# Optimization experiments

Hardware: AMD Instinct MI355X
Metric: run time of the kernel (lower is better)

## Reference

```python
import jax, jax.numpy as jnp
import numpy as np

N_NODES = 50000
N_EDGES = 800000
NODE_DIM = 64
MSG_DIM = 64
EDGE_DIM = 4
ROUNDS = 2


def setup_inputs() -> dict:
    key = jax.random.key(0)
    ks = jax.random.split(key, 10)
    in_dim = 2 * NODE_DIM + EDGE_DIM  # cat([src hv, dst hv, he])
    return {
        "hv": jax.random.normal(ks[0], (N_NODES, NODE_DIM), dtype=jnp.float32),
        "he": jax.random.uniform(ks[1], (N_EDGES, EDGE_DIM), dtype=jnp.float32),
        "W_msg": jax.random.normal(ks[2], (ROUNDS, in_dim, MSG_DIM), dtype=jnp.float32) * 0.05,
        "b_msg": jax.random.normal(ks[3], (ROUNDS, MSG_DIM), dtype=jnp.float32) * 0.05,
        "W_ih": jax.random.normal(ks[4], (ROUNDS, MSG_DIM, 3 * NODE_DIM), dtype=jnp.float32) * 0.05,
        "W_hh": jax.random.normal(ks[5], (ROUNDS, NODE_DIM, 3 * NODE_DIM), dtype=jnp.float32) * 0.05,
        "b_ih": jax.random.normal(ks[6], (ROUNDS, 3 * NODE_DIM), dtype=jnp.float32) * 0.05,
        "b_hh": jax.random.normal(ks[7], (ROUNDS, 3 * NODE_DIM), dtype=jnp.float32) * 0.05,
        "src": jax.random.randint(ks[8], (N_EDGES,), 0, N_NODES, dtype=jnp.int64)
        if jax.config.jax_enable_x64 else jax.random.randint(ks[8], (N_EDGES,), 0, N_NODES).astype(jnp.int32),
        "dst": jax.random.randint(ks[9], (N_EDGES,), 0, N_NODES).astype(jnp.int32),
    }


def gru_cell(a, h, W_ih, W_hh, b_ih, b_hh):
    # torch.nn.GRUCell math; gate order (r, z, n) along the 3H axis
    gi = a @ W_ih + b_ih   # [N, 3H]
    gh = h @ W_hh + b_hh   # [N, 3H]
    i_r, i_z, i_n = jnp.split(gi, 3, axis=1)
    h_r, h_z, h_n = jnp.split(gh, 3, axis=1)
    r = jax.nn.sigmoid(i_r + h_r)
    z = jax.nn.sigmoid(i_z + h_z)
    n = jnp.tanh(i_n + r * h_n)
    return (1.0 - z) * n + z * h


def reference(hv, he, W_msg, b_msg, W_ih, W_hh, b_ih, b_hh, src, dst):
    # GraphProp.forward: per-round gather -> message MLP -> scatter-sum -> GRU update
    N = hv.shape[0]
    src = src.astype(jnp.int32)
    dst = dst.astype(jnp.int32)
    rounds = W_msg.shape[0]
    for t in range(rounds):
        # dgmg_msg: m = cat([src hv, dst hv, he])  [E, 2*D+E_dim]
        m_in = jnp.concatenate([hv[src], hv[dst], he], axis=1)
        msg = m_in @ W_msg[t] + b_msg[t]  # message_funcs[t] (Linear + Identity)
        # dgmg_reduce: sum of inbound messages per destination node
        a = jax.ops.segment_sum(msg, dst, num_segments=N)  # [N, MSG_DIM]
        hv = gru_cell(a, hv, W_ih[t], W_hh[t], b_ih[t], b_hh[t])
    return hv
```

## Files before the change

kernel.cpp:

```cpp
#include <hip/hip_runtime.h>

#define N_NODES 50000
#define N_EDGES 800000
#define D 64
#define EDIM 4
#define IN_DIM 132
#define H3 192
#define PAD 72


__global__ void k_count(const int* __restrict__ dst, int* __restrict__ deg) {
    int e = blockIdx.x * blockDim.x + threadIdx.x;
    if (e < N_EDGES) atomicAdd(&deg[dst[e]], 1);
}

__global__ __launch_bounds__(256) void k_scan1(const int* __restrict__ deg,
                                               int* __restrict__ offsets,
                                               int* __restrict__ bsum) {
    __shared__ int sm[256];
    int tid = threadIdx.x;
    int i = blockIdx.x * 256 + tid;
    int x = (i < N_NODES) ? deg[i] : 0;
    sm[tid] = x;
    __syncthreads();
    for (int s = 1; s < 256; s <<= 1) {
        int v = (tid >= s) ? sm[tid - s] : 0;
        __syncthreads();
        sm[tid] += v;
        __syncthreads();
    }
    if (i < N_NODES) offsets[i] = sm[tid] - x;
    if (tid == 255) bsum[blockIdx.x] = sm[255];
}

__global__ __launch_bounds__(256) void k_scan2(const int* __restrict__ bsum,
                                               int* __restrict__ boff, int nblk) {
    __shared__ int sm[256];
    int tid = threadIdx.x;
    int x = (tid < nblk) ? bsum[tid] : 0;
    sm[tid] = x;
    __syncthreads();
    for (int s = 1; s < 256; s <<= 1) {
        int v = (tid >= s) ? sm[tid - s] : 0;
        __syncthreads();
        sm[tid] += v;
        __syncthreads();
    }
    if (tid < nblk) boff[tid] = sm[tid] - x;
}

__global__ __launch_bounds__(256) void k_scan3(int* __restrict__ offsets,
                                               const int* __restrict__ boff) {
    int i = blockIdx.x * 256 + threadIdx.x;
    if (i < N_NODES) offsets[i] += boff[blockIdx.x];
}

__global__ void k_fill(const int* __restrict__ src, const int* __restrict__ dst,
                       const int* __restrict__ offsets, int* __restrict__ cursor,
                       int* __restrict__ csr_src, int* __restrict__ csr_eid) {
    int e = blockIdx.x * blockDim.x + threadIdx.x;
    if (e < N_EDGES) {
        int d = dst[e];
        int pos = offsets[d] + atomicAdd(&cursor[d], 1);
        csr_src[pos] = src[e];
        csr_eid[pos] = e;
    }
}


template <int ROUND>
__global__ __launch_bounds__(256) void k_reduce(const float* __restrict__ hv,
                                                const float* __restrict__ he,
                                                const int* __restrict__ csr_src,
                                                const int* __restrict__ csr_eid,
                                                const int* __restrict__ offsets,
                                                const int* __restrict__ deg,
                                                float* __restrict__ S,
                                                float* __restrict__ Hsum) {
    int wave = (blockIdx.x * blockDim.x + threadIdx.x) >> 6;
    if (wave >= N_NODES) return;
    int lane = threadIdx.x & 63;
    int g = lane >> 4;
    int c = lane & 15;
    const int off = offsets[wave];
    const int cnt = deg[wave];
    float4 acc = make_float4(0.f, 0.f, 0.f, 0.f);
    float4 hacc = make_float4(0.f, 0.f, 0.f, 0.f);
    for (int e = g; e < cnt; e += 4) {
        int sn = csr_src[off + e];
        float4 v = ((const float4*)(hv + (size_t)sn * D))[c];
        acc.x += v.x; acc.y += v.y; acc.z += v.z; acc.w += v.w;
        if (ROUND == 0 && c == 0) {
            int eid = csr_eid[off + e];
            float4 h = *(const float4*)(he + (size_t)eid * EDIM);
            hacc.x += h.x; hacc.y += h.y; hacc.z += h.z; hacc.w += h.w;
        }
    }
    acc.x += __shfl_xor(acc.x, 16); acc.y += __shfl_xor(acc.y, 16);
    acc.z += __shfl_xor(acc.z, 16); acc.w += __shfl_xor(acc.w, 16);
    acc.x += __shfl_xor(acc.x, 32); acc.y += __shfl_xor(acc.y, 32);
    acc.z += __shfl_xor(acc.z, 32); acc.w += __shfl_xor(acc.w, 32);
    if (ROUND == 0) {
        hacc.x += __shfl_xor(hacc.x, 16); hacc.y += __shfl_xor(hacc.y, 16);
        hacc.z += __shfl_xor(hacc.z, 16); hacc.w += __shfl_xor(hacc.w, 16);
        hacc.x += __shfl_xor(hacc.x, 32); hacc.y += __shfl_xor(hacc.y, 32);
        hacc.z += __shfl_xor(hacc.z, 32); hacc.w += __shfl_xor(hacc.w, 32);
    }
    if (g == 0) ((float4*)(S + (size_t)wave * D))[c] = acc;
    if (ROUND == 0 && lane == 0) *(float4*)(Hsum + (size_t)wave * EDIM) = hacc;
}


__global__ __launch_bounds__(256) void k_node(const float* __restrict__ hv_in,
                                              const float* __restrict__ S,
                                              const float* __restrict__ Hsum,
                                              const int* __restrict__ deg,
                                              const float* __restrict__ W_msg,
                                              const float* __restrict__ b_msg,
                                              const float* __restrict__ W_ih,
                                              const float* __restrict__ W_hh,
                                              const float* __restrict__ b_ih,
                                              const float* __restrict__ b_hh,
                                              float* __restrict__ hv_out, int t) {
    __shared__ __align__(16) float XT[IN_DIM * PAD];
    __shared__ float degf_sm[64];

    const int tid = threadIdx.x;
    const int n_base = blockIdx.x * 64;

    {
        int nl = tid >> 2;
        int c4 = tid & 3;
        int n = n_base + nl;
        if (n >= N_NODES) n = N_NODES - 1;
        const float4* Srow = (const float4*)(S + (size_t)n * D);
        const float4* Hrow = (const float4*)(hv_in + (size_t)n * D);
#pragma unroll
        for (int i = 0; i < 4; ++i) {
            int k = c4 * 16 + i * 4;
            float4 sv = Srow[c4 * 4 + i];
            XT[(k + 0) * PAD + nl] = sv.x;
            XT[(k + 1) * PAD + nl] = sv.y;
            XT[(k + 2) * PAD + nl] = sv.z;
            XT[(k + 3) * PAD + nl] = sv.w;
            float4 hvv = Hrow[c4 * 4 + i];
            XT[(64 + k + 0) * PAD + nl] = hvv.x;
            XT[(64 + k + 1) * PAD + nl] = hvv.y;
            XT[(64 + k + 2) * PAD + nl] = hvv.z;
            XT[(64 + k + 3) * PAD + nl] = hvv.w;
        }
        if (c4 == 0) {
            float4 hs = *(const float4*)(Hsum + (size_t)n * EDIM);
            XT[(128) * PAD + nl] = hs.x;
            XT[(129) * PAD + nl] = hs.y;
            XT[(130) * PAD + nl] = hs.z;
            XT[(131) * PAD + nl] = hs.w;
        }
        if (c4 == 1) degf_sm[nl] = (float)deg[n];
    }
    __syncthreads();

    const int jg = tid & 15, ng = tid >> 4;
    const int n0 = ng * 4;
    const int j0 = jg * 4;

    float acc1[4][4], acc2[4][4];
#pragma unroll
    for (int a = 0; a < 4; ++a)
#pragma unroll
        for (int b = 0; b < 4; ++b) { acc1[a][b] = 0.f; acc2[a][b] = 0.f; }

    const float* Wm = W_msg + (size_t)t * IN_DIM * D;
#pragma unroll 4
    for (int k = 0; k < 64; ++k) {
        float4 A = *(const float4*)(&XT[k * PAD + n0]);
        float4 B = *(const float4*)(Wm + k * D + j0);
        float Aa[4] = {A.x, A.y, A.z, A.w};
        float Bb[4] = {B.x, B.y, B.z, B.w};
#pragma unroll
        for (int ni = 0; ni < 4; ++ni)
#pragma unroll
            for (int ji = 0; ji < 4; ++ji)
                acc1[ni][ji] = fmaf(Aa[ni], Bb[ji], acc1[ni][ji]);
    }
#pragma unroll 4
    for (int k = 64; k < 128; ++k) {
        float4 A = *(const float4*)(&XT[k * PAD + n0]);
        float4 B = *(const float4*)(Wm + k * D + j0);
        float Aa[4] = {A.x, A.y, A.z, A.w};
        float Bb[4] = {B.x, B.y, B.z, B.w};
#pragma unroll
        for (int ni = 0; ni < 4; ++ni)
#pragma unroll
            for (int ji = 0; ji < 4; ++ji)
                acc2[ni][ji] = fmaf(Aa[ni], Bb[ji], acc2[ni][ji]);
    }
#pragma unroll
    for (int k = 128; k < 132; ++k) {
        float4 A = *(const float4*)(&XT[k * PAD + n0]);
        float4 B = *(const float4*)(Wm + k * D + j0);
        float Aa[4] = {A.x, A.y, A.z, A.w};
        float Bb[4] = {B.x, B.y, B.z, B.w};
#pragma unroll
        for (int ni = 0; ni < 4; ++ni)
#pragma unroll
            for (int ji = 0; ji < 4; ++ji)
                acc1[ni][ji] = fmaf(Aa[ni], Bb[ji], acc1[ni][ji]);
    }

    float4 bm = *(const float4*)(b_msg + (size_t)t * D + j0);
    float bmv[4] = {bm.x, bm.y, bm.z, bm.w};
    float av[4][4];
#pragma unroll
    for (int ni = 0; ni < 4; ++ni) {
        float dg = degf_sm[n0 + ni];
#pragma unroll
        for (int ji = 0; ji < 4; ++ji)
            av[ni][ji] = acc1[ni][ji] + dg * (acc2[ni][ji] + bmv[ji]);
    }
    __syncthreads();
#pragma unroll
    for (int ni = 0; ni < 4; ++ni)
#pragma unroll
        for (int ji = 0; ji < 4; ++ji)
            XT[(j0 + ji) * PAD + (n0 + ni)] = av[ni][ji];
    __syncthreads();

    const float* Wi = W_ih + (size_t)t * D * H3;
    const float* Wh = W_hh + (size_t)t * D * H3;
    const float* bi = b_ih + (size_t)t * H3;
    const float* bh = b_hh + (size_t)t * H3;

    float4 biR = *(const float4*)(bi + j0);
    float4 biZ = *(const float4*)(bi + 64 + j0);
    float4 biN = *(const float4*)(bi + 128 + j0);
    float4 bhR = *(const float4*)(bh + j0);
    float4 bhZ = *(const float4*)(bh + 64 + j0);
    float4 bhN = *(const float4*)(bh + 128 + j0);
    float accR[4][4], accZ[4][4], accIN[4][4], accHN[4][4];
    {
        float r0[4] = {biR.x + bhR.x, biR.y + bhR.y, biR.z + bhR.z, biR.w + bhR.w};
        float z0[4] = {biZ.x + bhZ.x, biZ.y + bhZ.y, biZ.z + bhZ.z, biZ.w + bhZ.w};
        float in0[4] = {biN.x, biN.y, biN.z, biN.w};
        float hn0[4] = {bhN.x, bhN.y, bhN.z, bhN.w};
#pragma unroll
        for (int ni = 0; ni < 4; ++ni)
#pragma unroll
            for (int ji = 0; ji < 4; ++ji) {
                accR[ni][ji] = r0[ji];
                accZ[ni][ji] = z0[ji];
                accIN[ni][ji] = in0[ji];
                accHN[ni][ji] = hn0[ji];
            }
    }

#pragma unroll 2
    for (int k = 0; k < 64; ++k) {
        float4 A = *(const float4*)(&XT[k * PAD + n0]);
        const float* wrow = Wi + k * H3;
        float4 wR = *(const float4*)(wrow + j0);
        float4 wZ = *(const float4*)(wrow + 64 + j0);
        float4 wN = *(const float4*)(wrow + 128 + j0);
        float Aa[4] = {A.x, A.y, A.z, A.w};
        float R[4] = {wR.x, wR.y, wR.z, wR.w};
        float Z[4] = {wZ.x, wZ.y, wZ.z, wZ.w};
        float Nn[4] = {wN.x, wN.y, wN.z, wN.w};
#pragma unroll
        for (int ni = 0; ni < 4; ++ni)
#pragma unroll
            for (int ji = 0; ji < 4; ++ji) {
                accR[ni][ji] = fmaf(Aa[ni], R[ji], accR[ni][ji]);
                accZ[ni][ji] = fmaf(Aa[ni], Z[ji], accZ[ni][ji]);
                accIN[ni][ji] = fmaf(Aa[ni], Nn[ji], accIN[ni][ji]);
            }
    }
#pragma unroll 2
    for (int k = 0; k < 64; ++k) {
        float4 A = *(const float4*)(&XT[(64 + k) * PAD + n0]);
        const float* wrow = Wh + k * H3;
        float4 wR = *(const float4*)(wrow + j0);
        float4 wZ = *(const float4*)(wrow + 64 + j0);
        float4 wN = *(const float4*)(wrow + 128 + j0);
        float Aa[4] = {A.x, A.y, A.z, A.w};
        float R[4] = {wR.x, wR.y, wR.z, wR.w};
        float Z[4] = {wZ.x, wZ.y, wZ.z, wZ.w};
        float Nn[4] = {wN.x, wN.y, wN.z, wN.w};
#pragma unroll
        for (int ni = 0; ni < 4; ++ni)
#pragma unroll
            for (int ji = 0; ji < 4; ++ji) {
                accR[ni][ji] = fmaf(Aa[ni], R[ji], accR[ni][ji]);
                accZ[ni][ji] = fmaf(Aa[ni], Z[ji], accZ[ni][ji]);
                accHN[ni][ji] = fmaf(Aa[ni], Nn[ji], accHN[ni][ji]);
            }
    }

#pragma unroll
    for (int ni = 0; ni < 4; ++ni) {
        int n = n_base + n0 + ni;
        if (n < N_NODES) {
            float4 hv4 = *(const float4*)(hv_in + (size_t)n * D + j0);
            float hvv[4] = {hv4.x, hv4.y, hv4.z, hv4.w};
            float o[4];
#pragma unroll
            for (int ji = 0; ji < 4; ++ji) {
                float r = 1.f / (1.f + __expf(-accR[ni][ji]));
                float z = 1.f / (1.f + __expf(-accZ[ni][ji]));
                float nin = accIN[ni][ji] + r * accHN[ni][ji];
                float nn = 2.f / (1.f + __expf(-2.f * nin)) - 1.f;
                o[ji] = (1.f - z) * nn + z * hvv[ji];
            }
            *(float4*)(hv_out + (size_t)n * D + j0) = make_float4(o[0], o[1], o[2], o[3]);
        }
    }
}


extern "C" void kernel_launch(void* const* d_in, const int* in_sizes, int n_in,
                              void* d_out, int out_size, void* d_ws, size_t ws_size,
                              hipStream_t stream) {
    const float* hv = (const float*)d_in[0];
    const float* he = (const float*)d_in[1];
    const float* W_msg = (const float*)d_in[2];
    const float* b_msg = (const float*)d_in[3];
    const float* W_ih = (const float*)d_in[4];
    const float* W_hh = (const float*)d_in[5];
    const float* b_ih = (const float*)d_in[6];
    const float* b_hh = (const float*)d_in[7];
    const int* src = (const int*)d_in[8];
    const int* dst = (const int*)d_in[9];
    float* out = (float*)d_out;

    char* p = (char*)d_ws;
    int* deg = (int*)p;        p += (size_t)N_NODES * sizeof(int);
    int* cursor = (int*)p;     p += (size_t)N_NODES * sizeof(int);
    int* offsets = (int*)p;    p += (size_t)N_NODES * sizeof(int);
    int* bsum = (int*)p;       p += 256 * sizeof(int);
    int* boff = (int*)p;       p += 256 * sizeof(int);
    int* csr_src = (int*)p;    p += (size_t)N_EDGES * sizeof(int);
    float* Hsum = (float*)p;   p += (size_t)N_NODES * EDIM * sizeof(float);
    float* S = (float*)p;      p += (size_t)N_NODES * D * sizeof(float);
    float* hv_buf = (float*)p; p += (size_t)N_NODES * D * sizeof(float);
    int* csr_eid = (int*)hv_buf;

    const int NBLK = (N_NODES + 255) / 256;

    hipMemsetAsync(deg, 0, N_NODES * sizeof(int), stream);
    hipMemsetAsync(cursor, 0, N_NODES * sizeof(int), stream);

    k_count<<<(N_EDGES + 255) / 256, 256, 0, stream>>>(dst, deg);
    k_scan1<<<NBLK, 256, 0, stream>>>(deg, offsets, bsum);
    k_scan2<<<1, 256, 0, stream>>>(bsum, boff, NBLK);
    k_scan3<<<NBLK, 256, 0, stream>>>(offsets, boff);
    k_fill<<<(N_EDGES + 255) / 256, 256, 0, stream>>>(src, dst, offsets, cursor, csr_src, csr_eid);

    const int RBLK = (N_NODES * 64 + 255) / 256;
    const int GBLK = (N_NODES + 63) / 64;

    k_reduce<0><<<RBLK, 256, 0, stream>>>(hv, he, csr_src, csr_eid, offsets, deg, S, Hsum);
    k_node<<<GBLK, 256, 0, stream>>>(hv, S, Hsum, deg, W_msg, b_msg, W_ih, W_hh, b_ih, b_hh, hv_buf, 0);

    k_reduce<1><<<RBLK, 256, 0, stream>>>(hv_buf, he, csr_src, csr_eid, offsets, deg, S, Hsum);
    k_node<<<GBLK, 256, 0, stream>>>(hv_buf, S, Hsum, deg, W_msg, b_msg, W_ih, W_hh, b_ih, b_hh, out, 1);
}
```

Baseline: 429.8 us.

## Remap node kernel to one node per lane with wave-uniform weight columns

```diff
diff --git a/kernel.cpp b/kernel.cpp
--- a/kernel.cpp
+++ b/kernel.cpp
@@ -6,7 +6,6 @@
 #define EDIM 4
 #define IN_DIM 132
 #define H3 192
-#define PAD 72
 
 
 __global__ void k_count(const int* __restrict__ dst, int* __restrict__ deg) {
@@ -111,7 +110,7 @@
 }
 
 
-__global__ __launch_bounds__(256) void k_node(const float* __restrict__ hv_in,
+__global__ __launch_bounds__(512) void k_node(const float* __restrict__ hv_in,
                                               const float* __restrict__ S,
                                               const float* __restrict__ Hsum,
                                               const int* __restrict__ deg,
@@ -122,196 +121,132 @@
                                               const float* __restrict__ b_ih,
                                               const float* __restrict__ b_hh,
                                               float* __restrict__ hv_out, int t) {
-    __shared__ __align__(16) float XT[IN_DIM * PAD];
-    __shared__ float degf_sm[64];
+    __shared__ float XT[IN_DIM * D];
 
     const int tid = threadIdx.x;
-    const int n_base = blockIdx.x * 64;
+    const int n_base = blockIdx.x * D;
 
     {
-        int nl = tid >> 2;
-        int c4 = tid & 3;
+        int nl = tid >> 3;
+        int c = tid & 7;
         int n = n_base + nl;
         if (n >= N_NODES) n = N_NODES - 1;
-        const float4* Srow = (const float4*)(S + (size_t)n * D);
-        const float4* Hrow = (const float4*)(hv_in + (size_t)n * D);
-#pragma unroll
-        for (int i = 0; i < 4; ++i) {
-            int k = c4 * 16 + i * 4;
-            float4 sv = Srow[c4 * 4 + i];
-            XT[(k + 0) * PAD + nl] = sv.x;
-            XT[(k + 1) * PAD + nl] = sv.y;
-            XT[(k + 2) * PAD + nl] = sv.z;
-            XT[(k + 3) * PAD + nl] = sv.w;
-            float4 hvv = Hrow[c4 * 4 + i];
-            XT[(64 + k + 0) * PAD + nl] = hvv.x;
-            XT[(64 + k + 1) * PAD + nl] = hvv.y;
-            XT[(64 + k + 2) * PAD + nl] = hvv.z;
-            XT[(64 + k + 3) * PAD + nl] = hvv.w;
-        }
-        if (c4 == 0) {
+        const float4* Sp = (const float4*)(S + (size_t)n * D);
+        const float4* Hp = (const float4*)(hv_in + (size_t)n * D);
+        float4 s0 = Sp[c * 2], s1 = Sp[c * 2 + 1];
+        float4 h0 = Hp[c * 2], h1 = Hp[c * 2 + 1];
+        int k0 = c * 8;
+        XT[(k0 + 0) * D + nl] = s0.x; XT[(k0 + 1) * D + nl] = s0.y;
+        XT[(k0 + 2) * D + nl] = s0.z; XT[(k0 + 3) * D + nl] = s0.w;
+        XT[(k0 + 4) * D + nl] = s1.x; XT[(k0 + 5) * D + nl] = s1.y;
+        XT[(k0 + 6) * D + nl] = s1.z; XT[(k0 + 7) * D + nl] = s1.w;
+        XT[(64 + k0 + 0) * D + nl] = h0.x; XT[(64 + k0 + 1) * D + nl] = h0.y;
+        XT[(64 + k0 + 2) * D + nl] = h0.z; XT[(64 + k0 + 3) * D + nl] = h0.w;
+        XT[(64 + k0 + 4) * D + nl] = h1.x; XT[(64 + k0 + 5) * D + nl] = h1.y;
+        XT[(64 + k0 + 6) * D + nl] = h1.z; XT[(64 + k0 + 7) * D + nl] = h1.w;
+        if (c == 0) {
             float4 hs = *(const float4*)(Hsum + (size_t)n * EDIM);
-            XT[(128) * PAD + nl] = hs.x;
-            XT[(129) * PAD + nl] = hs.y;
-            XT[(130) * PAD + nl] = hs.z;
-            XT[(131) * PAD + nl] = hs.w;
-        }
-        if (c4 == 1) degf_sm[nl] = (float)deg[n];
-    }
-    __syncthreads();
-
-    const int jg = tid & 15, ng = tid >> 4;
-    const int n0 = ng * 4;
-    const int j0 = jg * 4;
-
-    float acc1[4][4], acc2[4][4];
-#pragma unroll
-    for (int a = 0; a < 4; ++a)
-#pragma unroll
-        for (int b = 0; b < 4; ++b) { acc1[a][b] = 0.f; acc2[a][b] = 0.f; }
-
-    const float* Wm = W_msg + (size_t)t * IN_DIM * D;
+            XT[128 * D + nl] = hs.x; XT[129 * D + nl] = hs.y;
+            XT[130 * D + nl] = hs.z; XT[131 * D + nl] = hs.w;
+        }
+    }
+    __syncthreads();
+
+    const int lane = tid & 63;
+    const int w = __builtin_amdgcn_readfirstlane(tid) >> 6;
+    const int jb = w * 8;
+    const int n = n_base + lane;
+    const bool nvalid = (n < N_NODES);
+    const int nc = nvalid ? n : N_NODES - 1;
+    const float degf = (float)deg[nc];
+
+    const float* __restrict__ Wm = W_msg + (size_t)t * IN_DIM * D;
+
+    float acc1[8], acc2[8];
+#pragma unroll
+    for (int i = 0; i < 8; ++i) { acc1[i] = 0.f; acc2[i] = 0.f; }
+
 #pragma unroll 4
     for (int k = 0; k < 64; ++k) {
-        float4 A = *(const float4*)(&XT[k * PAD + n0]);
-        float4 B = *(const float4*)(Wm + k * D + j0);
-        float Aa[4] = {A.x, A.y, A.z, A.w};
-        float Bb[4] = {B.x, B.y, B.z, B.w};
-#pragma unroll
-        for (int ni = 0; ni < 4; ++ni)
-#pragma unroll
-            for (int ji = 0; ji < 4; ++ji)
-                acc1[ni][ji] = fmaf(Aa[ni], Bb[ji], acc1[ni][ji]);
-    }
-#pragma unroll 4
-    for (int k = 64; k < 128; ++k) {
-        float4 A = *(const float4*)(&XT[k * PAD + n0]);
-        float4 B = *(const float4*)(Wm + k * D + j0);
-        float Aa[4] = {A.x, A.y, A.z, A.w};
-        float Bb[4] = {B.x, B.y, B.z, B.w};
-#pragma unroll
-        for (int ni = 0; ni < 4; ++ni)
-#pragma unroll
-            for (int ji = 0; ji < 4; ++ji)
-                acc2[ni][ji] = fmaf(Aa[ni], Bb[ji], acc2[ni][ji]);
-    }
-#pragma unroll
-    for (int k = 128; k < 132; ++k) {
-        float4 A = *(const float4*)(&XT[k * PAD + n0]);
-        float4 B = *(const float4*)(Wm + k * D + j0);
-        float Aa[4] = {A.x, A.y, A.z, A.w};
-        float Bb[4] = {B.x, B.y, B.z, B.w};
-#pragma unroll
-        for (int ni = 0; ni < 4; ++ni)
-#pragma unroll
-            for (int ji = 0; ji < 4; ++ji)
-                acc1[ni][ji] = fmaf(Aa[ni], Bb[ji], acc1[ni][ji]);
-    }
-
-    float4 bm = *(const float4*)(b_msg + (size_t)t * D + j0);
-    float bmv[4] = {bm.x, bm.y, bm.z, bm.w};
-    float av[4][4];
-#pragma unroll
-    for (int ni = 0; ni < 4; ++ni) {
-        float dg = degf_sm[n0 + ni];
-#pragma unroll
-        for (int ji = 0; ji < 4; ++ji)
-            av[ni][ji] = acc1[ni][ji] + dg * (acc2[ni][ji] + bmv[ji]);
-    }
-    __syncthreads();
-#pragma unroll
-    for (int ni = 0; ni < 4; ++ni)
-#pragma unroll
-        for (int ji = 0; ji < 4; ++ji)
-            XT[(j0 + ji) * PAD + (n0 + ni)] = av[ni][ji];
-    __syncthreads();
-
-    const float* Wi = W_ih + (size_t)t * D * H3;
-    const float* Wh = W_hh + (size_t)t * D * H3;
+        float aS = XT[k * D + lane];
+        float aH = XT[(64 + k) * D + lane];
+        const float* wr1 = Wm + k * D + jb;
+        const float* wr2 = Wm + (64 + k) * D + jb;
+#pragma unroll
+        for (int i = 0; i < 8; ++i) {
+            acc1[i] = fmaf(aS, wr1[i], acc1[i]);
+            acc2[i] = fmaf(aH, wr2[i], acc2[i]);
+        }
+    }
+#pragma unroll
+    for (int q = 0; q < 4; ++q) {
+        float aQ = XT[(128 + q) * D + lane];
+        const float* wr = Wm + (128 + q) * D + jb;
+#pragma unroll
+        for (int i = 0; i < 8; ++i) acc1[i] = fmaf(aQ, wr[i], acc1[i]);
+    }
+
+    const float* bmp = b_msg + (size_t)t * D + jb;
+    float av[8];
+#pragma unroll
+    for (int i = 0; i < 8; ++i) av[i] = acc1[i] + degf * (acc2[i] + bmp[i]);
+
+    __syncthreads();
+#pragma unroll
+    for (int i = 0; i < 8; ++i) XT[(jb + i) * D + lane] = av[i];
+    __syncthreads();
+
+    const float* __restrict__ Wi = W_ih + (size_t)t * D * H3;
+    const float* __restrict__ Wh = W_hh + (size_t)t * D * H3;
     const float* bi = b_ih + (size_t)t * H3;
     const float* bh = b_hh + (size_t)t * H3;
 
-    float4 biR = *(const float4*)(bi + j0);
-    float4 biZ = *(const float4*)(bi + 64 + j0);
-    float4 biN = *(const float4*)(bi + 128 + j0);
-    float4 bhR = *(const float4*)(bh + j0);
-    float4 bhZ = *(const float4*)(bh + 64 + j0);
-    float4 bhN = *(const float4*)(bh + 128 + j0);
-    float accR[4][4], accZ[4][4], accIN[4][4], accHN[4][4];
-    {
-        float r0[4] = {biR.x + bhR.x, biR.y + bhR.y, biR.z + bhR.z, biR.w + bhR.w};
-        float z0[4] = {biZ.x + bhZ.x, biZ.y + bhZ.y, biZ.z + bhZ.z, biZ.w + bhZ.w};
-        float in0[4] = {biN.x, biN.y, biN.z, biN.w};
-        float hn0[4] = {bhN.x, bhN.y, bhN.z, bhN.w};
-#pragma unroll
-        for (int ni = 0; ni < 4; ++ni)
-#pragma unroll
-            for (int ji = 0; ji < 4; ++ji) {
-                accR[ni][ji] = r0[ji];
-                accZ[ni][ji] = z0[ji];
-                accIN[ni][ji] = in0[ji];
-                accHN[ni][ji] = hn0[ji];
-            }
-    }
-
-#pragma unroll 2
+    float aR[8], aZ[8], aN[8], aHN[8];
+#pragma unroll
+    for (int i = 0; i < 8; ++i) {
+        aR[i] = bi[jb + i] + bh[jb + i];
+        aZ[i] = bi[64 + jb + i] + bh[64 + jb + i];
+        aN[i] = bi[128 + jb + i];
+        aHN[i] = bh[128 + jb + i];
+    }
+
+#pragma unroll 4
     for (int k = 0; k < 64; ++k) {
-        float4 A = *(const float4*)(&XT[k * PAD + n0]);
-        const float* wrow = Wi + k * H3;
-        float4 wR = *(const float4*)(wrow + j0);
-        float4 wZ = *(const float4*)(wrow + 64 + j0);
-        float4 wN = *(const float4*)(wrow + 128 + j0);
-        float Aa[4] = {A.x, A.y, A.z, A.w};
-        float R[4] = {wR.x, wR.y, wR.z, wR.w};
-        float Z[4] = {wZ.x, wZ.y, wZ.z, wZ.w};
-        float Nn[4] = {wN.x, wN.y, wN.z, wN.w};
-#pragma unroll
-        for (int ni = 0; ni < 4; ++ni)
-#pragma unroll
-            for (int ji = 0; ji < 4; ++ji) {
-                accR[ni][ji] = fmaf(Aa[ni], R[ji], accR[ni][ji]);
-                accZ[ni][ji] = fmaf(Aa[ni], Z[ji], accZ[ni][ji]);
-                accIN[ni][ji] = fmaf(Aa[ni], Nn[ji], accIN[ni][ji]);
-            }
-    }
-#pragma unroll 2
+        float Aa = XT[k * D + lane];
+        const float* wr = Wi + k * H3;
+#pragma unroll
+        for (int i = 0; i < 8; ++i) {
+            aR[i] = fmaf(Aa, wr[jb + i], aR[i]);
+            aZ[i] = fmaf(Aa, wr[64 + jb + i], aZ[i]);
+            aN[i] = fmaf(Aa, wr[128 + jb + i], aN[i]);
+        }
+    }
+#pragma unroll 4
     for (int k = 0; k < 64; ++k) {
-        float4 A = *(const float4*)(&XT[(64 + k) * PAD + n0]);
-        const float* wrow = Wh + k * H3;
-        float4 wR = *(const float4*)(wrow + j0);
-        float4 wZ = *(const float4*)(wrow + 64 + j0);
-        float4 wN = *(const float4*)(wrow + 128 + j0);
-        float Aa[4] = {A.x, A.y, A.z, A.w};
-        float R[4] = {wR.x, wR.y, wR.z, wR.w};
-        float Z[4] = {wZ.x, wZ.y, wZ.z, wZ.w};
-        float Nn[4] = {wN.x, wN.y, wN.z, wN.w};
-#pragma unroll
-        for (int ni = 0; ni < 4; ++ni)
-#pragma unroll
-            for (int ji = 0; ji < 4; ++ji) {
-                accR[ni][ji] = fmaf(Aa[ni], R[ji], accR[ni][ji]);
-                accZ[ni][ji] = fmaf(Aa[ni], Z[ji], accZ[ni][ji]);
-                accHN[ni][ji] = fmaf(Aa[ni], Nn[ji], accHN[ni][ji]);
-            }
-    }
-
-#pragma unroll
-    for (int ni = 0; ni < 4; ++ni) {
-        int n = n_base + n0 + ni;
-        if (n < N_NODES) {
-            float4 hv4 = *(const float4*)(hv_in + (size_t)n * D + j0);
-            float hvv[4] = {hv4.x, hv4.y, hv4.z, hv4.w};
-            float o[4];
-#pragma unroll
-            for (int ji = 0; ji < 4; ++ji) {
-                float r = 1.f / (1.f + __expf(-accR[ni][ji]));
-                float z = 1.f / (1.f + __expf(-accZ[ni][ji]));
-                float nin = accIN[ni][ji] + r * accHN[ni][ji];
-                float nn = 2.f / (1.f + __expf(-2.f * nin)) - 1.f;
-                o[ji] = (1.f - z) * nn + z * hvv[ji];
-            }
-            *(float4*)(hv_out + (size_t)n * D + j0) = make_float4(o[0], o[1], o[2], o[3]);
-        }
+        float Ah = XT[(64 + k) * D + lane];
+        const float* wr = Wh + k * H3;
+#pragma unroll
+        for (int i = 0; i < 8; ++i) {
+            aR[i] = fmaf(Ah, wr[jb + i], aR[i]);
+            aZ[i] = fmaf(Ah, wr[64 + jb + i], aZ[i]);
+            aHN[i] = fmaf(Ah, wr[128 + jb + i], aHN[i]);
+        }
+    }
+
+    float o[8];
+#pragma unroll
+    for (int i = 0; i < 8; ++i) {
+        float r = 1.f / (1.f + __expf(-aR[i]));
+        float z = 1.f / (1.f + __expf(-aZ[i]));
+        float nin = aN[i] + r * aHN[i];
+        float nn = 2.f / (1.f + __expf(-2.f * nin)) - 1.f;
+        float hold = XT[(64 + jb + i) * D + lane];
+        o[i] = (1.f - z) * nn + z * hold;
+    }
+    if (nvalid) {
+        float4* op = (float4*)(hv_out + (size_t)n * D + jb);
+        op[0] = make_float4(o[0], o[1], o[2], o[3]);
+        op[1] = make_float4(o[4], o[5], o[6], o[7]);
     }
 }
 
@@ -358,8 +293,8 @@
     const int GBLK = (N_NODES + 63) / 64;
 
     k_reduce<0><<<RBLK, 256, 0, stream>>>(hv, he, csr_src, csr_eid, offsets, deg, S, Hsum);
-    k_node<<<GBLK, 256, 0, stream>>>(hv, S, Hsum, deg, W_msg, b_msg, W_ih, W_hh, b_ih, b_hh, hv_buf, 0);
+    k_node<<<GBLK, 512, 0, stream>>>(hv, S, Hsum, deg, W_msg, b_msg, W_ih, W_hh, b_ih, b_hh, hv_buf, 0);
 
     k_reduce<1><<<RBLK, 256, 0, stream>>>(hv_buf, he, csr_src, csr_eid, offsets, deg, S, Hsum);
-    k_node<<<GBLK, 256, 0, stream>>>(hv_buf, S, Hsum, deg, W_msg, b_msg, W_ih, W_hh, b_ih, b_hh, out, 1);
-}
+    k_node<<<GBLK, 512, 0, stream>>>(hv_buf, S, Hsum, deg, W_msg, b_msg, W_ih, W_hh, b_ih, b_hh, out, 1);
+}
```

Measured after the change: 432.7 us. No clear change (+0.7%).
